# Kernel tuning notes

Measured on AMD Instinct MI355X. Metric: run time of the kernel, lower is better.

Reference implementation:

```python
import jax, jax.numpy as jnp
import numpy as np

B, S, D, H = 8, 1024, 512, 8
HD = D // H
NEG = -1000000000.0
LN_EPS = 1e-5


def setup_inputs() -> dict:
    key = jax.random.key(0)
    ks = jax.random.split(key, 16)
    sc = 0.02
    inp = {
        "query": jax.random.normal(ks[0], (B, S, D), jnp.float32),
        "inputs": jax.random.normal(ks[1], (B, S, D), jnp.float32),
        "ren_mat": jax.random.uniform(ks[2], (B, S, S), jnp.float32) * 5.0,
        "timestamp": jax.random.normal(ks[3], (B, S, S), jnp.float32),
        # causal mask: True where attention is disallowed (strictly upper triangular)
        "mask": jnp.triu(jnp.ones((1, S, S), jnp.bool_), k=1),
        "Wq": jax.random.normal(ks[4], (D, D), jnp.float32) * sc,
        "bq": jnp.zeros((D,), jnp.float32),
        "Wk": jax.random.normal(ks[5], (D, D), jnp.float32) * sc,
        "bk": jnp.zeros((D,), jnp.float32),
        "Wv": jax.random.normal(ks[6], (D, D), jnp.float32) * sc,
        "bv": jnp.zeros((D,), jnp.float32),
        "Wo": jax.random.normal(ks[7], (D, D), jnp.float32) * sc,
        "bo": jnp.zeros((D,), jnp.float32),
        "W1": jax.random.normal(ks[8], (D, D), jnp.float32) * sc,
        "b1": jnp.zeros((D,), jnp.float32),
        "ln_g": jnp.ones((D,), jnp.float32),
        "ln_b": jnp.zeros((D,), jnp.float32),
        "l1": jax.random.uniform(ks[9], (1,), jnp.float32),
    }
    return inp


def reference(query, inputs, ren_mat, timestamp, mask,
              Wq, bq, Wk, bk, Wv, bv, Wo, bo, W1, b1, ln_g, ln_b, l1):
    # QKV projections (qk_same=False path; q,k,v all computed from `inputs`)
    def proj(x, W, b):
        return (x @ W.T + b).reshape(B, S, H, HD).transpose(0, 2, 1, 3)  # (B,H,S,HD)

    q = proj(inputs, Wq, bq)
    k = proj(inputs, Wk, bk)
    v = proj(inputs, Wv, bv)

    m = mask[:, None]  # (1,1,S,S), broadcasts over batch & heads

    scores = jnp.einsum("bhqd,bhkd->bhqk", q, k) / jnp.sqrt(jnp.float32(HD))
    scores = jnp.where(m, NEG, scores)
    prob_attn = jax.nn.softmax(scores, axis=-1)

    # memory blend: log10(ren+1) and exp(-|t|), each masked, summed, softmaxed
    ren_feat = jnp.where(m, NEG, jnp.log10(ren_mat + 1.0)[:, None])      # (B,H,S,S)
    time_stamp = jnp.where(m, NEG, jnp.exp(-jnp.abs(timestamp))[:, None])
    mem_attn = jax.nn.softmax(ren_feat + time_stamp, axis=-1)

    l = l1  # (1,) learned blend coefficient
    prob_attn = (1.0 - l) * prob_attn + l * mem_attn

    out = jnp.einsum("bhqk,bhkd->bhqd", prob_attn, v)
    out = out.transpose(0, 2, 1, 3).reshape(B, S, D)
    out = out @ Wo.T + bo

    # residual FFN + layernorm (dropout disabled / eval mode)
    out = out + (out @ W1.T + b1)
    mu = jnp.mean(out, axis=-1, keepdims=True)
    var = jnp.var(out, axis=-1, keepdims=True)
    out = (out - mu) / jnp.sqrt(var + LN_EPS) * ln_g + ln_b
    return out
```

## Files before the change

### kernel.cpp

```cpp
#include <hip/hip_runtime.h>
#include <math.h>

constexpr int kB = 8, kS = 1024, kD = 512, kH = 8, kHD = 64;
constexpr int kM = kB * kS;

typedef __attribute__((ext_vector_type(8))) short s8v;
typedef __attribute__((ext_vector_type(4))) float f4v;
typedef __attribute__((ext_vector_type(4))) unsigned short u4v;

__device__ __forceinline__ unsigned short f2bf(float f) {
    union { float f; unsigned int u; } c; c.f = f;
    unsigned int u = c.u + 0x7FFFu + ((c.u >> 16) & 1u);
    return (unsigned short)(u >> 16);
}

__device__ __forceinline__ void gl2lds(const unsigned short* g, unsigned short* l) {
    __builtin_amdgcn_global_load_lds(
        (const __attribute__((address_space(1))) unsigned int*)g,
        (__attribute__((address_space(3))) unsigned int*)l, 16, 0, 0);
}

__global__ __launch_bounds__(256) void prep_kernel(
    const float* __restrict__ X, const float* __restrict__ Wq,
    const float* __restrict__ Wk, const float* __restrict__ Wv,
    const float* __restrict__ Wo, const float* __restrict__ W1,
    const float* __restrict__ ren, const float* __restrict__ ts,
    unsigned short* __restrict__ Xbf, unsigned short* __restrict__ Wqkv,
    unsigned short* __restrict__ Wobf, unsigned short* __restrict__ W1bf,
    unsigned short* __restrict__ mem)
{
    __shared__ float red[4];
    const int t = threadIdx.x;
    if (blockIdx.x < 5376) {
        const int idx = blockIdx.x * 256 + t;
        const float* src; unsigned short* dst; int off; bool isw1 = false;
        if (idx < 1048576)      { src = X;  dst = Xbf;           off = idx; }
        else if (idx < 1114112) { src = Wq; dst = Wqkv;          off = idx - 1048576; }
        else if (idx < 1179648) { src = Wk; dst = Wqkv + 262144; off = idx - 1114112; }
        else if (idx < 1245184) { src = Wv; dst = Wqkv + 524288; off = idx - 1179648; }
        else if (idx < 1310720) { src = Wo; dst = Wobf;          off = idx - 1245184; }
        else                    { src = W1; dst = W1bf;          off = idx - 1310720; isw1 = true; }
        float4 v = ((const float4*)src)[off];
        if (isw1) {
            const int e0 = off * 4;
            const int row = e0 >> 9, col0 = e0 & 511;
            if (row >= col0 && row < col0 + 4) ((float*)&v)[row - col0] += 1.0f;
        }
        u4v p;
        p[0] = f2bf(v.x); p[1] = f2bf(v.y); p[2] = f2bf(v.z); p[3] = f2bf(v.w);
        ((u4v*)dst)[off] = p;
        return;
    }
    const int bi = blockIdx.x - 5376;
    const int i = bi & (kS - 1);
    const float* renr = ren + (size_t)bi * kS;
    const float* tsr  = ts  + (size_t)bi * kS;
    unsigned short* memr = mem + (size_t)bi * kS;
    const int j0 = t * 4;
    const float4 r4 = *(const float4*)(renr + j0);
    const float4 t4 = *(const float4*)(tsr + j0);
    float rv[4] = {r4.x, r4.y, r4.z, r4.w};
    float tv[4] = {t4.x, t4.y, t4.z, t4.w};
    float p4[4];
    float lsum = 0.0f;
#pragma unroll
    for (int e = 0; e < 4; ++e) {
        const int j = j0 + e;
        float p = 0.0f;
        if (j <= i) {
            const float val = 0.30102999566f * __log2f(rv[e] + 1.0f) + __expf(-fabsf(tv[e]));
            p = __expf(val);
        }
        p4[e] = p;
        lsum += p;
    }
#pragma unroll
    for (int d = 1; d < 64; d <<= 1) lsum += __shfl_xor(lsum, d);
    if ((t & 63) == 0) red[t >> 6] = lsum;
    __syncthreads();
    const float Z = red[0] + red[1] + red[2] + red[3];
    const float inv = 1.0f / Z;
    u4v pk;
#pragma unroll
    for (int e = 0; e < 4; ++e) pk[e] = f2bf(p4[e] * inv);
    *(u4v*)(memr + j0) = pk;
}

template <int NT>
__device__ __forceinline__ void mfma_core2(
    const unsigned short* __restrict__ A, const unsigned short* __restrict__ B,
    int M0, int N0, unsigned short* As, unsigned short* Bs, f4v (&acc)[4][NT])
{
    const int t = threadIdx.x, w = t >> 6, lane = t & 63;
    const int l16 = lane & 15, quad = lane >> 4;
    const int wm = (w & 1) * 64, wn = (w >> 1) * (NT * 16);
    constexpr int NB = NT / 2;

    const unsigned short* gA[2]; unsigned short* lA[2];
#pragma unroll
    for (int i = 0; i < 2; ++i) {
        const int r0 = w * 32 + i * 16;
        const int r = r0 + (lane >> 2);
        const int c = (lane & 3) ^ ((r >> 1) & 3);
        gA[i] = A + (size_t)(M0 + r) * 512 + c * 8;
        lA[i] = As + r0 * 32;
    }
    const unsigned short* gB[NB]; unsigned short* lB[NB];
#pragma unroll
    for (int i = 0; i < NB; ++i) {
        const int r0 = w * (16 * NB) + i * 16;
        const int r = r0 + (lane >> 2);
        const int c = (lane & 3) ^ ((r >> 1) & 3);
        gB[i] = B + (size_t)(N0 + r) * 512 + c * 8;
        lB[i] = Bs + r0 * 32;
    }

    const f4v zero = {0.0f, 0.0f, 0.0f, 0.0f};
#pragma unroll
    for (int mt = 0; mt < 4; ++mt)
#pragma unroll
        for (int nt = 0; nt < NT; ++nt) acc[mt][nt] = zero;

#pragma unroll 1
    for (int k0 = 0; k0 < 512; k0 += 32) {
        gl2lds(gA[0] + k0, lA[0]);
        gl2lds(gA[1] + k0, lA[1]);
#pragma unroll
        for (int i = 0; i < NB; ++i) gl2lds(gB[i] + k0, lB[i]);
        __syncthreads();
        s8v af[4], bf_[NT];
#pragma unroll
        for (int mt = 0; mt < 4; ++mt) {
            const int r = wm + mt * 16 + l16;
            const int p = r * 4 + (quad ^ ((r >> 1) & 3));
            af[mt] = *(const s8v*)&As[p * 8];
        }
#pragma unroll
        for (int nt = 0; nt < NT; ++nt) {
            const int r = wn + nt * 16 + l16;
            const int p = r * 4 + (quad ^ ((r >> 1) & 3));
            bf_[nt] = *(const s8v*)&Bs[p * 8];
        }
#pragma unroll
        for (int mt = 0; mt < 4; ++mt)
#pragma unroll
            for (int nt = 0; nt < NT; ++nt)
                acc[mt][nt] = __builtin_amdgcn_mfma_f32_16x16x32_bf16(
                    af[mt], bf_[nt], acc[mt][nt], 0, 0, 0);
        __syncthreads();
    }
}

__global__ __launch_bounds__(256) void qkv_mfma_kernel(
    const unsigned short* __restrict__ Xbf, const unsigned short* __restrict__ Wqkv,
    const float* __restrict__ bq, const float* __restrict__ bk, const float* __restrict__ bv,
    unsigned short* __restrict__ qbf, unsigned short* __restrict__ kbf,
    unsigned short* __restrict__ vTbf)
{
    __shared__ __align__(16) unsigned short As[128 * 32];
    __shared__ __align__(16) unsigned short Bs[128 * 32];
    f4v acc[4][4];
    const int y = blockIdx.y;
    const int t = threadIdx.x, w = t >> 6, lane = t & 63;
    const int l16 = lane & 15, quad = lane >> 4;
    const int wm = (w & 1) * 64, wn = (w >> 1) * 64;

    if (y < 8) {
        const int M0 = blockIdx.x * 128, N0 = y * 128;
        mfma_core2<4>(Xbf, Wqkv, M0, N0, As, Bs, acc);
        const int z = N0 >> 9;
        const float* bias = (z == 0) ? bq : bk;
        unsigned short* out = (z == 0) ? qbf : kbf;
#pragma unroll
        for (int nt = 0; nt < 4; ++nt) {
            const int n512 = (N0 + wn + nt * 16 + l16) & 511;
            const int h = n512 >> 6, hd = n512 & 63;
            const float bv_ = bias[n512];
#pragma unroll
            for (int mt = 0; mt < 4; ++mt) {
#pragma unroll
                for (int rr = 0; rr < 4; ++rr) {
                    const int m = M0 + wm + mt * 16 + quad * 4 + rr;
                    const int b = m >> 10, s = m & (kS - 1);
                    out[(((size_t)b * kH + h) * kS + s) * kHD + hd] =
                        f2bf(acc[mt][nt][rr] + bv_);
                }
            }
        }
    } else {
        const int M0 = (y - 8) * 128, N0 = blockIdx.x * 128;
        mfma_core2<4>(Wqkv + (size_t)1024 * 512, Xbf, M0, N0, As, Bs, acc);
#pragma unroll
        for (int mt = 0; mt < 4; ++mt) {
#pragma unroll
            for (int rr = 0; rr < 4; ++rr) {
                const int vcol = M0 + wm + mt * 16 + quad * 4 + rr;
                const int h = vcol >> 6, hd = vcol & 63;
                const float bv_ = bv[vcol];
#pragma unroll
                for (int nt = 0; nt < 4; ++nt) {
                    const int sg = N0 + wn + nt * 16 + l16;
                    const int b = sg >> 10, s = sg & (kS - 1);
                    vTbf[(((size_t)b * kH + h) * kHD + hd) * kS + s] =
                        f2bf(acc[mt][nt][rr] + bv_);
                }
            }
        }
    }
}

__global__ __launch_bounds__(256) void gemm_wo_kernel(
    const unsigned short* __restrict__ Abf, const unsigned short* __restrict__ Wobf,
    const float* __restrict__ bo, unsigned short* __restrict__ out1bf)
{
    __shared__ __align__(16) unsigned short As[128 * 32];
    __shared__ __align__(16) unsigned short Bs[64 * 32];
    f4v acc[4][2];
    const int M0 = blockIdx.x * 128, N0 = blockIdx.y * 64;
    mfma_core2<2>(Abf, Wobf, M0, N0, As, Bs, acc);
    const int t = threadIdx.x, w = t >> 6, lane = t & 63;
    const int l16 = lane & 15, quad = lane >> 4;
    const int wm = (w & 1) * 64, wn = (w >> 1) * 32;
#pragma unroll
    for (int nt = 0; nt < 2; ++nt) {
        const int n = N0 + wn + nt * 16 + l16;
        const float bv_ = bo[n];
#pragma unroll
        for (int mt = 0; mt < 4; ++mt)
#pragma unroll
            for (int rr = 0; rr < 4; ++rr) {
                const int m = M0 + wm + mt * 16 + quad * 4 + rr;
                out1bf[(size_t)m * kD + n] = f2bf(acc[mt][nt][rr] + bv_);
            }
    }
}

__global__ __launch_bounds__(256) void gemm_w1_kernel(
    const unsigned short* __restrict__ Abf, const unsigned short* __restrict__ W1bf,
    const float* __restrict__ b1, float* __restrict__ out)
{
    __shared__ __align__(16) unsigned short As[128 * 32];
    __shared__ __align__(16) unsigned short Bs[64 * 32];
    f4v acc[4][2];
    const int M0 = blockIdx.x * 128, N0 = blockIdx.y * 64;
    mfma_core2<2>(Abf, W1bf, M0, N0, As, Bs, acc);
    const int t = threadIdx.x, w = t >> 6, lane = t & 63;
    const int l16 = lane & 15, quad = lane >> 4;
    const int wm = (w & 1) * 64, wn = (w >> 1) * 32;
#pragma unroll
    for (int nt = 0; nt < 2; ++nt) {
        const int n = N0 + wn + nt * 16 + l16;
        const float bv_ = b1[n];
#pragma unroll
        for (int mt = 0; mt < 4; ++mt)
#pragma unroll
            for (int rr = 0; rr < 4; ++rr) {
                const int m = M0 + wm + mt * 16 + quad * 4 + rr;
                out[(size_t)m * kD + n] = acc[mt][nt][rr] + bv_;
            }
    }
}

#define LDSFRAG(tile, r, c) (*(const s8v*)&(tile)[(size_t)(r) * 64 + ((((c) ^ ((r) & 7))) << 3)])

__global__ __launch_bounds__(256) void flash_attn_kernel(
    const unsigned short* __restrict__ q, const unsigned short* __restrict__ k,
    const unsigned short* __restrict__ vT, const unsigned short* __restrict__ mem,
    const float* __restrict__ l1, unsigned short* __restrict__ aout)
{
    const int qp = blockIdx.x;
    const int hi = 15 - qp, lo = qp;
    const int h = blockIdx.y, b = blockIdx.z;
    const int bh = b * kH + h;
    const int t = threadIdx.x;
    const int w = t >> 6, lane = t & 63;
    const int quad = lane >> 4, l16 = lane & 15;
    const float lam = l1[0];

    __shared__ __align__(16) unsigned short KV[2][2][64 * 64];
    __shared__ __align__(16) unsigned short P_lds[4][16][72];

    const int tbase[2] = {hi * 64, lo * 64};
    s8v qa[2][2];
    const unsigned short* mbase[2];
#pragma unroll
    for (int ti = 0; ti < 2; ++ti) {
        const unsigned short* qrow = q + ((size_t)bh * kS + tbase[ti] + w * 16 + l16) * kHD;
        qa[ti][0] = *(const s8v*)(qrow + quad * 8);
        qa[ti][1] = *(const s8v*)(qrow + 32 + quad * 8);
        mbase[ti] = mem + ((size_t)b * kS + tbase[ti] + w * 16 + l16) * kS;
    }

    const unsigned short* kb = k + (size_t)bh * kS * kHD;
    const unsigned short* vb = vT + (size_t)bh * kHD * kS;

    const unsigned short* gsrc[4];
    int gstep[4];
    unsigned short* ldst[4];
#pragma unroll
    for (int u = 0; u < 4; ++u) {
        const int s = w * 4 + u;
        const int rloc = (s & 7) * 8 + (lane >> 3);
        const int chunk = (lane & 7) ^ ((lane >> 3) & 7);
        if (s < 8) {
            gsrc[u] = kb + (size_t)rloc * kHD + chunk * 8;
            gstep[u] = kHD;
            ldst[u] = &KV[0][0][(size_t)s * 512];
        } else {
            gsrc[u] = vb + (size_t)rloc * kS + chunk * 8;
            gstep[u] = 1;
            ldst[u] = &KV[0][1][(size_t)(s - 8) * 512];
        }
    }

#pragma unroll
    for (int u = 0; u < 4; ++u) gl2lds(gsrc[u], ldst[u]);
    s8v maC[2][2];
#pragma unroll
    for (int ti = 0; ti < 2; ++ti) {
        maC[ti][0] = *(const s8v*)(mbase[ti] + quad * 8);
        maC[ti][1] = *(const s8v*)(mbase[ti] + 32 + quad * 8);
    }

    const f4v zero = {0.0f, 0.0f, 0.0f, 0.0f};
    f4v Oa[2][4], Om[2][4];
    float lr[2][4];
#pragma unroll
    for (int ti = 0; ti < 2; ++ti)
#pragma unroll
        for (int nt = 0; nt < 4; ++nt) {
            Oa[ti][nt] = zero; Om[ti][nt] = zero; lr[ti][nt] = 0.0f;
        }

    for (int kt = 0; kt <= hi; ++kt) {
        __syncthreads();
        const int cur = kt & 1;
        s8v maN[2][2];
        const bool stage_next = (kt < hi);
        if (stage_next) {
            const int jn = (kt + 1) * 64;
            const int boff = ((kt + 1) & 1) * 8192;
#pragma unroll
            for (int u = 0; u < 4; ++u)
                gl2lds(gsrc[u] + (size_t)jn * gstep[u], ldst[u] + boff);
            maN[0][0] = *(const s8v*)(mbase[0] + jn + quad * 8);
            maN[0][1] = *(const s8v*)(mbase[0] + jn + 32 + quad * 8);
            if (kt + 1 <= lo) {
                maN[1][0] = *(const s8v*)(mbase[1] + jn + quad * 8);
                maN[1][1] = *(const s8v*)(mbase[1] + jn + 32 + quad * 8);
            }
        }
        const unsigned short* Kc = &KV[cur][0][0];
        const unsigned short* Vc = &KV[cur][1][0];

        s8v vf[4][2];
#pragma unroll
        for (int nt = 0; nt < 4; ++nt) {
            const int r = nt * 16 + l16;
            vf[nt][0] = LDSFRAG(Vc, r, quad);
            vf[nt][1] = LDSFRAG(Vc, r, 4 + quad);
        }

#pragma unroll
        for (int ti = 0; ti < 2; ++ti) {
            if (ti == 1 && kt > lo) continue;
            const bool diag = (kt == ((ti == 0) ? hi : lo));
#pragma unroll
            for (int ct = 0; ct < 4; ++ct) {
                const int r = ct * 16 + l16;
                const s8v kb0 = LDSFRAG(Kc, r, quad);
                const s8v kb1 = LDSFRAG(Kc, r, 4 + quad);
                f4v acc = zero;
                acc = __builtin_amdgcn_mfma_f32_16x16x32_bf16(qa[ti][0], kb0, acc, 0, 0, 0);
                acc = __builtin_amdgcn_mfma_f32_16x16x32_bf16(qa[ti][1], kb1, acc, 0, 0, 0);
#pragma unroll
                for (int rr = 0; rr < 4; ++rr) {
                    float p = __expf(acc[rr] * 0.125f);
                    if (diag && (ct * 16 + l16) > (w * 16 + quad * 4 + rr)) p = 0.0f;
                    lr[ti][rr] += p;
                    P_lds[w][quad * 4 + rr][ct * 16 + l16] = f2bf(p);
                }
            }
            const s8v pa0 = *(const s8v*)&P_lds[w][l16][quad * 8];
            const s8v pa1 = *(const s8v*)&P_lds[w][l16][32 + quad * 8];
#pragma unroll
            for (int nt = 0; nt < 4; ++nt) {
                Oa[ti][nt] = __builtin_amdgcn_mfma_f32_16x16x32_bf16(pa0, vf[nt][0], Oa[ti][nt], 0, 0, 0);
                Oa[ti][nt] = __builtin_amdgcn_mfma_f32_16x16x32_bf16(pa1, vf[nt][1], Oa[ti][nt], 0, 0, 0);
                Om[ti][nt] = __builtin_amdgcn_mfma_f32_16x16x32_bf16(maC[ti][0], vf[nt][0], Om[ti][nt], 0, 0, 0);
                Om[ti][nt] = __builtin_amdgcn_mfma_f32_16x16x32_bf16(maC[ti][1], vf[nt][1], Om[ti][nt], 0, 0, 0);
            }
        }
        if (stage_next) {
            maC[0][0] = maN[0][0]; maC[0][1] = maN[0][1];
            if (kt + 1 <= lo) { maC[1][0] = maN[1][0]; maC[1][1] = maN[1][1]; }
        }
    }

#pragma unroll
    for (int ti = 0; ti < 2; ++ti) {
        float inv[4];
#pragma unroll
        for (int rr = 0; rr < 4; ++rr) {
            float Z = lr[ti][rr];
            Z += __shfl_xor(Z, 1);
            Z += __shfl_xor(Z, 2);
            Z += __shfl_xor(Z, 4);
            Z += __shfl_xor(Z, 8);
            inv[rr] = (1.0f - lam) / Z;
        }
        const int r0 = tbase[ti] + w * 16;
#pragma unroll
        for (int nt = 0; nt < 4; ++nt)
#pragma unroll
            for (int rr = 0; rr < 4; ++rr) {
                const int i = r0 + quad * 4 + rr;
                const int d = h * kHD + nt * 16 + l16;
                aout[((size_t)b * kS + i) * kD + d] =
                    f2bf(Oa[ti][nt][rr] * inv[rr] + lam * Om[ti][nt][rr]);
            }
    }
}

__global__ __launch_bounds__(256) void ln_kernel(
    const float* __restrict__ x, const float* __restrict__ g,
    const float* __restrict__ bb, float* __restrict__ out)
{
    const int row = blockIdx.x;
    const int t = threadIdx.x;
    const float* xr = x + (size_t)row * kD;
    float a = xr[t], c = xr[t + 256];
    __shared__ float red[256];
    float s1 = a + c, s2 = a * a + c * c;
    red[t] = s1;
    __syncthreads();
    for (int s = 128; s > 0; s >>= 1) {
        if (t < s) red[t] += red[t + s];
        __syncthreads();
    }
    const float sum = red[0];
    __syncthreads();
    red[t] = s2;
    __syncthreads();
    for (int s = 128; s > 0; s >>= 1) {
        if (t < s) red[t] += red[t + s];
        __syncthreads();
    }
    const float sq = red[0];
    float mu = sum * (1.0f / kD);
    float var = sq * (1.0f / kD) - mu * mu;
    float inv = rsqrtf(var + 1e-5f);
    out[(size_t)row * kD + t]       = (a - mu) * inv * g[t] + bb[t];
    out[(size_t)row * kD + t + 256] = (c - mu) * inv * g[t + 256] + bb[t + 256];
}

extern "C" void kernel_launch(void* const* d_in, const int* in_sizes, int n_in,
                              void* d_out, int out_size, void* d_ws, size_t ws_size,
                              hipStream_t stream) {
    const float* X   = (const float*)d_in[1];
    const float* ren = (const float*)d_in[2];
    const float* ts  = (const float*)d_in[3];
    const float* Wq = (const float*)d_in[5];  const float* bq = (const float*)d_in[6];
    const float* Wk = (const float*)d_in[7];  const float* bk = (const float*)d_in[8];
    const float* Wv = (const float*)d_in[9];  const float* bv = (const float*)d_in[10];
    const float* Wo = (const float*)d_in[11]; const float* bo = (const float*)d_in[12];
    const float* W1 = (const float*)d_in[13]; const float* b1 = (const float*)d_in[14];
    const float* lng = (const float*)d_in[15]; const float* lnb = (const float*)d_in[16];
    const float* l1 = (const float*)d_in[17];
    float* out = (float*)d_out;

    char* wsb = (char*)d_ws;
    unsigned short* Xbf    = (unsigned short*)(wsb);
    unsigned short* Wqkvbf = (unsigned short*)(wsb + (8u  << 20));
    unsigned short* Wobf   = (unsigned short*)(wsb + (10u << 20));
    unsigned short* W1bf   = (unsigned short*)(wsb + (11u << 20));
    unsigned short* qbf    = (unsigned short*)(wsb + (12u << 20));
    unsigned short* kbf    = (unsigned short*)(wsb + (20u << 20));
    unsigned short* vTbf   = (unsigned short*)(wsb + (28u << 20));
    unsigned short* membf  = (unsigned short*)(wsb + (36u << 20));
    unsigned short* aoutbf = (unsigned short*)(wsb + (52u << 20));
    unsigned short* out1bf = (unsigned short*)(wsb + (60u << 20));

    prep_kernel<<<dim3(5376 + kB * kS), 256, 0, stream>>>(
        X, Wq, Wk, Wv, Wo, W1, ren, ts, Xbf, Wqkvbf, Wobf, W1bf, membf);
    qkv_mfma_kernel<<<dim3(kM / 128, 12), 256, 0, stream>>>(
        Xbf, Wqkvbf, bq, bk, bv, qbf, kbf, vTbf);
    flash_attn_kernel<<<dim3(8, kH, kB), 256, 0, stream>>>(
        qbf, kbf, vTbf, membf, l1, aoutbf);
    gemm_wo_kernel<<<dim3(kM / 128, kD / 64), 256, 0, stream>>>(
        aoutbf, Wobf, bo, out1bf);
    gemm_w1_kernel<<<dim3(kM / 128, kD / 64), 256, 0, stream>>>(
        out1bf, W1bf, b1, out);
    ln_kernel<<<dim3(kM), 256, 0, stream>>>(out, lng, lnb, out);
}
```

Measured before the change: 283.6 us.

## Fold Wo into W1 algebraically and split attention key loop across wave groups

Precomputes the combined weight (W1+I)·Wo and its bias inside the QKV launch, so the two back-to-back output GEMMs become one GEMM. This removes one GEMM launch and the bf16 round trip of the intermediate activation, at the cost of an extra small weight GEMM and a Wo transpose in prep. Separately, the flash attention kernel goes to 512 threads, with two wave groups each handling alternate key tiles over a 4-deep LDS buffer. Their partial accumulators and row sums are then reduced through LDS, adding parallelism per block but also extra synchronisation and LDS traffic.

```diff
diff --git a/kernel.cpp b/kernel.cpp
--- a/kernel.cpp
+++ b/kernel.cpp
@@ -25,21 +25,21 @@
     const float* __restrict__ Wk, const float* __restrict__ Wv,
     const float* __restrict__ Wo, const float* __restrict__ W1,
     const float* __restrict__ ren, const float* __restrict__ ts,
+    const float* __restrict__ bo_g,
     unsigned short* __restrict__ Xbf, unsigned short* __restrict__ Wqkv,
-    unsigned short* __restrict__ Wobf, unsigned short* __restrict__ W1bf,
+    unsigned short* __restrict__ WoT, unsigned short* __restrict__ W1bf,
     unsigned short* __restrict__ mem)
 {
     __shared__ float red[4];
     const int t = threadIdx.x;
-    if (blockIdx.x < 5376) {
+    if (blockIdx.x < 5120) {
         const int idx = blockIdx.x * 256 + t;
         const float* src; unsigned short* dst; int off; bool isw1 = false;
         if (idx < 1048576)      { src = X;  dst = Xbf;           off = idx; }
         else if (idx < 1114112) { src = Wq; dst = Wqkv;          off = idx - 1048576; }
         else if (idx < 1179648) { src = Wk; dst = Wqkv + 262144; off = idx - 1114112; }
         else if (idx < 1245184) { src = Wv; dst = Wqkv + 524288; off = idx - 1179648; }
-        else if (idx < 1310720) { src = Wo; dst = Wobf;          off = idx - 1245184; }
-        else                    { src = W1; dst = W1bf;          off = idx - 1310720; isw1 = true; }
+        else                    { src = W1; dst = W1bf;          off = idx - 1245184; isw1 = true; }
         float4 v = ((const float4*)src)[off];
         if (isw1) {
             const int e0 = off * 4;
@@ -51,7 +51,34 @@
         ((u4v*)dst)[off] = p;
         return;
     }
-    const int bi = blockIdx.x - 5376;
+    if (blockIdx.x >= 13312) {
+        const int bi2 = blockIdx.x - 13312;
+        if (bi2 < 64) {
+            __shared__ float T[64][65];
+            const int tr = bi2 >> 3, tc = bi2 & 7;
+            const int rr0 = t >> 4, cc0 = (t & 15) * 4;
+#pragma unroll
+            for (int i2 = 0; i2 < 4; ++i2) {
+                const int r = i2 * 16 + rr0;
+                const float4 v = *(const float4*)&Wo[(size_t)(tr * 64 + r) * 512 + tc * 64 + cc0];
+                T[r][cc0] = v.x; T[r][cc0 + 1] = v.y; T[r][cc0 + 2] = v.z; T[r][cc0 + 3] = v.w;
+            }
+            __syncthreads();
+#pragma unroll
+            for (int i2 = 0; i2 < 4; ++i2) {
+                const int r2 = i2 * 16 + rr0;
+                u4v p;
+                p[0] = f2bf(T[cc0][r2]);     p[1] = f2bf(T[cc0 + 1][r2]);
+                p[2] = f2bf(T[cc0 + 2][r2]); p[3] = f2bf(T[cc0 + 3][r2]);
+                *(u4v*)&WoT[(size_t)(tc * 64 + r2) * 512 + tr * 64 + cc0] = p;
+            }
+        } else {
+            WoT[262144 + t]       = f2bf(bo_g[t]);
+            WoT[262144 + 256 + t] = f2bf(bo_g[t + 256]);
+        }
+        return;
+    }
+    const int bi = blockIdx.x - 5120;
     const int i = bi & (kS - 1);
     const float* renr = ren + (size_t)bi * kS;
     const float* tsr  = ts  + (size_t)bi * kS;
@@ -154,17 +181,41 @@
 __global__ __launch_bounds__(256) void qkv_mfma_kernel(
     const unsigned short* __restrict__ Xbf, const unsigned short* __restrict__ Wqkv,
     const float* __restrict__ bq, const float* __restrict__ bk, const float* __restrict__ bv,
+    const unsigned short* __restrict__ W1bf, const unsigned short* __restrict__ WoT,
+    const float* __restrict__ b1,
     unsigned short* __restrict__ qbf, unsigned short* __restrict__ kbf,
-    unsigned short* __restrict__ vTbf)
+    unsigned short* __restrict__ vTbf,
+    unsigned short* __restrict__ Wcomb, float* __restrict__ bcomb)
 {
     __shared__ __align__(16) unsigned short As[128 * 32];
     __shared__ __align__(16) unsigned short Bs[128 * 32];
-    f4v acc[4][4];
     const int y = blockIdx.y;
     const int t = threadIdx.x, w = t >> 6, lane = t & 63;
     const int l16 = lane & 15, quad = lane >> 4;
+
+    if (y == 12) {
+        if (blockIdx.x >= 36) return;
+        f4v acc[4][2];
+        const int M0 = (blockIdx.x / 9) * 128, N0 = (blockIdx.x % 9) * 64;
+        mfma_core2<2>(W1bf, WoT, M0, N0, As, Bs, acc);
+        const int wm = (w & 1) * 64, wn = (w >> 1) * 32;
+#pragma unroll
+        for (int nt = 0; nt < 2; ++nt) {
+            const int qq = N0 + wn + nt * 16 + l16;
+#pragma unroll
+            for (int mt = 0; mt < 4; ++mt)
+#pragma unroll
+                for (int rr = 0; rr < 4; ++rr) {
+                    const int m = M0 + wm + mt * 16 + quad * 4 + rr;
+                    if (qq < 512)       Wcomb[(size_t)m * 512 + qq] = f2bf(acc[mt][nt][rr]);
+                    else if (qq == 512) bcomb[m] = acc[mt][nt][rr] + b1[m];
+                }
+        }
+        return;
+    }
+
+    f4v acc[4][4];
     const int wm = (w & 1) * 64, wn = (w >> 1) * 64;
-
     if (y < 8) {
         const int M0 = blockIdx.x * 128, N0 = y * 128;
         mfma_core2<4>(Xbf, Wqkv, M0, N0, As, Bs, acc);
@@ -209,48 +260,22 @@
     }
 }
 
-__global__ __launch_bounds__(256) void gemm_wo_kernel(
-    const unsigned short* __restrict__ Abf, const unsigned short* __restrict__ Wobf,
-    const float* __restrict__ bo, unsigned short* __restrict__ out1bf)
+__global__ __launch_bounds__(256) void gemm_final_kernel(
+    const unsigned short* __restrict__ Abf, const unsigned short* __restrict__ Wcomb,
+    const float* __restrict__ bcomb, float* __restrict__ out)
 {
     __shared__ __align__(16) unsigned short As[128 * 32];
     __shared__ __align__(16) unsigned short Bs[64 * 32];
     f4v acc[4][2];
     const int M0 = blockIdx.x * 128, N0 = blockIdx.y * 64;
-    mfma_core2<2>(Abf, Wobf, M0, N0, As, Bs, acc);
+    mfma_core2<2>(Abf, Wcomb, M0, N0, As, Bs, acc);
     const int t = threadIdx.x, w = t >> 6, lane = t & 63;
     const int l16 = lane & 15, quad = lane >> 4;
     const int wm = (w & 1) * 64, wn = (w >> 1) * 32;
 #pragma unroll
     for (int nt = 0; nt < 2; ++nt) {
         const int n = N0 + wn + nt * 16 + l16;
-        const float bv_ = bo[n];
-#pragma unroll
-        for (int mt = 0; mt < 4; ++mt)
-#pragma unroll
-            for (int rr = 0; rr < 4; ++rr) {
-                const int m = M0 + wm + mt * 16 + quad * 4 + rr;
-                out1bf[(size_t)m * kD + n] = f2bf(acc[mt][nt][rr] + bv_);
-            }
-    }
-}
-
-__global__ __launch_bounds__(256) void gemm_w1_kernel(
-    const unsigned short* __restrict__ Abf, const unsigned short* __restrict__ W1bf,
-    const float* __restrict__ b1, float* __restrict__ out)
-{
-    __shared__ __align__(16) unsigned short As[128 * 32];
-    __shared__ __align__(16) unsigned short Bs[64 * 32];
-    f4v acc[4][2];
-    const int M0 = blockIdx.x * 128, N0 = blockIdx.y * 64;
-    mfma_core2<2>(Abf, W1bf, M0, N0, As, Bs, acc);
-    const int t = threadIdx.x, w = t >> 6, lane = t & 63;
-    const int l16 = lane & 15, quad = lane >> 4;
-    const int wm = (w & 1) * 64, wn = (w >> 1) * 32;
-#pragma unroll
-    for (int nt = 0; nt < 2; ++nt) {
-        const int n = N0 + wn + nt * 16 + l16;
-        const float bv_ = b1[n];
+        const float bv_ = bcomb[n];
 #pragma unroll
         for (int mt = 0; mt < 4; ++mt)
 #pragma unroll
@@ -263,7 +288,7 @@
 
 #define LDSFRAG(tile, r, c) (*(const s8v*)&(tile)[(size_t)(r) * 64 + ((((c) ^ ((r) & 7))) << 3)])
 
-__global__ __launch_bounds__(256) void flash_attn_kernel(
+__global__ __launch_bounds__(512, 4) void flash_attn_kernel(
     const unsigned short* __restrict__ q, const unsigned short* __restrict__ k,
     const unsigned short* __restrict__ vT, const unsigned short* __restrict__ mem,
     const float* __restrict__ l1, unsigned short* __restrict__ aout)
@@ -273,54 +298,43 @@
     const int h = blockIdx.y, b = blockIdx.z;
     const int bh = b * kH + h;
     const int t = threadIdx.x;
-    const int w = t >> 6, lane = t & 63;
+    const int w = t >> 6, w4 = w & 3, g = w >> 2;
+    const int lane = t & 63;
     const int quad = lane >> 4, l16 = lane & 15;
     const float lam = l1[0];
 
-    __shared__ __align__(16) unsigned short KV[2][2][64 * 64];
-    __shared__ __align__(16) unsigned short P_lds[4][16][72];
+    __shared__ __align__(16) unsigned short KV[4][2][64 * 64];
+    __shared__ __align__(16) unsigned short P_lds[8][16 * 64];
 
     const int tbase[2] = {hi * 64, lo * 64};
     s8v qa[2][2];
     const unsigned short* mbase[2];
 #pragma unroll
     for (int ti = 0; ti < 2; ++ti) {
-        const unsigned short* qrow = q + ((size_t)bh * kS + tbase[ti] + w * 16 + l16) * kHD;
+        const unsigned short* qrow = q + ((size_t)bh * kS + tbase[ti] + w4 * 16 + l16) * kHD;
         qa[ti][0] = *(const s8v*)(qrow + quad * 8);
         qa[ti][1] = *(const s8v*)(qrow + 32 + quad * 8);
-        mbase[ti] = mem + ((size_t)b * kS + tbase[ti] + w * 16 + l16) * kS;
+        mbase[ti] = mem + ((size_t)b * kS + tbase[ti] + w4 * 16 + l16) * kS;
     }
 
     const unsigned short* kb = k + (size_t)bh * kS * kHD;
     const unsigned short* vb = vT + (size_t)bh * kHD * kS;
 
     const unsigned short* gsrc[4];
-    int gstep[4];
-    unsigned short* ldst[4];
+    int gstep[4], loff[4];
 #pragma unroll
     for (int u = 0; u < 4; ++u) {
-        const int s = w * 4 + u;
-        const int rloc = (s & 7) * 8 + (lane >> 3);
+        const int sp = w4 * 4 + u;
+        const int rloc = (sp & 7) * 8 + (lane >> 3);
         const int chunk = (lane & 7) ^ ((lane >> 3) & 7);
-        if (s < 8) {
-            gsrc[u] = kb + (size_t)rloc * kHD + chunk * 8;
-            gstep[u] = kHD;
-            ldst[u] = &KV[0][0][(size_t)s * 512];
-        } else {
-            gsrc[u] = vb + (size_t)rloc * kS + chunk * 8;
-            gstep[u] = 1;
-            ldst[u] = &KV[0][1][(size_t)(s - 8) * 512];
-        }
-    }
-
-#pragma unroll
-    for (int u = 0; u < 4; ++u) gl2lds(gsrc[u], ldst[u]);
-    s8v maC[2][2];
-#pragma unroll
-    for (int ti = 0; ti < 2; ++ti) {
-        maC[ti][0] = *(const s8v*)(mbase[ti] + quad * 8);
-        maC[ti][1] = *(const s8v*)(mbase[ti] + 32 + quad * 8);
-    }
+        if (sp < 8) { gsrc[u] = kb + (size_t)rloc * kHD + chunk * 8; gstep[u] = 64 * kHD; loff[u] = (sp & 7) * 512; }
+        else        { gsrc[u] = vb + (size_t)rloc * kS  + chunk * 8; gstep[u] = 64;       loff[u] = 4096 + (sp & 7) * 512; }
+    }
+    unsigned short* KVf = &KV[0][0][0];
+
+#pragma unroll
+    for (int u = 0; u < 4; ++u)
+        gl2lds(gsrc[u] + (size_t)g * gstep[u], KVf + g * 8192 + loff[u]);
 
     const f4v zero = {0.0f, 0.0f, 0.0f, 0.0f};
     f4v Oa[2][4], Om[2][4];
@@ -332,26 +346,30 @@
             Oa[ti][nt] = zero; Om[ti][nt] = zero; lr[ti][nt] = 0.0f;
         }
 
-    for (int kt = 0; kt <= hi; ++kt) {
-        __syncthreads();
-        const int cur = kt & 1;
-        s8v maN[2][2];
-        const bool stage_next = (kt < hi);
-        if (stage_next) {
-            const int jn = (kt + 1) * 64;
-            const int boff = ((kt + 1) & 1) * 8192;
+    const int nI = hi / 2 + 1;
+    for (int it = 0; it < nI; ++it) {
+        __syncthreads();
+        const int kt = 2 * it + g;
+        const int Tn = 2 * it + 2 + g;
+        if (Tn <= hi) {
 #pragma unroll
             for (int u = 0; u < 4; ++u)
-                gl2lds(gsrc[u] + (size_t)jn * gstep[u], ldst[u] + boff);
-            maN[0][0] = *(const s8v*)(mbase[0] + jn + quad * 8);
-            maN[0][1] = *(const s8v*)(mbase[0] + jn + 32 + quad * 8);
-            if (kt + 1 <= lo) {
-                maN[1][0] = *(const s8v*)(mbase[1] + jn + quad * 8);
-                maN[1][1] = *(const s8v*)(mbase[1] + jn + 32 + quad * 8);
-            }
-        }
-        const unsigned short* Kc = &KV[cur][0][0];
-        const unsigned short* Vc = &KV[cur][1][0];
+                gl2lds(gsrc[u] + (size_t)Tn * gstep[u], KVf + (Tn & 3) * 8192 + loff[u]);
+        }
+        const bool a0 = (kt <= hi);
+        const bool a1 = (kt <= lo);
+        if (!a0) continue;
+
+        const int jn = kt * 64;
+        s8v ma0a, ma0b, ma1a, ma1b;
+        ma0a = *(const s8v*)(mbase[0] + jn + quad * 8);
+        ma0b = *(const s8v*)(mbase[0] + jn + 32 + quad * 8);
+        if (a1) {
+            ma1a = *(const s8v*)(mbase[1] + jn + quad * 8);
+            ma1b = *(const s8v*)(mbase[1] + jn + 32 + quad * 8);
+        }
+        const unsigned short* Kc = &KV[kt & 3][0][0];
+        const unsigned short* Vc = &KV[kt & 3][1][0];
 
         s8v vf[4][2];
 #pragma unroll
@@ -363,7 +381,7 @@
 
 #pragma unroll
         for (int ti = 0; ti < 2; ++ti) {
-            if (ti == 1 && kt > lo) continue;
+            if (ti == 1 && !a1) continue;
             const bool diag = (kt == ((ti == 0) ? hi : lo));
 #pragma unroll
             for (int ct = 0; ct < 4; ++ct) {
@@ -376,25 +394,67 @@
 #pragma unroll
                 for (int rr = 0; rr < 4; ++rr) {
                     float p = __expf(acc[rr] * 0.125f);
-                    if (diag && (ct * 16 + l16) > (w * 16 + quad * 4 + rr)) p = 0.0f;
+                    if (diag && r > (w4 * 16 + quad * 4 + rr)) p = 0.0f;
                     lr[ti][rr] += p;
-                    P_lds[w][quad * 4 + rr][ct * 16 + l16] = f2bf(p);
+                    const int pr = quad * 4 + rr;
+                    P_lds[w][pr * 64 + ((((ct * 2 + (l16 >> 3)) ^ (pr & 7)) << 3) | (l16 & 7))] = f2bf(p);
                 }
             }
-            const s8v pa0 = *(const s8v*)&P_lds[w][l16][quad * 8];
-            const s8v pa1 = *(const s8v*)&P_lds[w][l16][32 + quad * 8];
+            const s8v pa0 = LDSFRAG(&P_lds[w][0], l16, quad);
+            const s8v pa1 = LDSFRAG(&P_lds[w][0], l16, 4 + quad);
+            const s8v m0 = (ti == 0) ? ma0a : ma1a;
+            const s8v m1 = (ti == 0) ? ma0b : ma1b;
 #pragma unroll
             for (int nt = 0; nt < 4; ++nt) {
                 Oa[ti][nt] = __builtin_amdgcn_mfma_f32_16x16x32_bf16(pa0, vf[nt][0], Oa[ti][nt], 0, 0, 0);
                 Oa[ti][nt] = __builtin_amdgcn_mfma_f32_16x16x32_bf16(pa1, vf[nt][1], Oa[ti][nt], 0, 0, 0);
-                Om[ti][nt] = __builtin_amdgcn_mfma_f32_16x16x32_bf16(maC[ti][0], vf[nt][0], Om[ti][nt], 0, 0, 0);
-                Om[ti][nt] = __builtin_amdgcn_mfma_f32_16x16x32_bf16(maC[ti][1], vf[nt][1], Om[ti][nt], 0, 0, 0);
-            }
-        }
-        if (stage_next) {
-            maC[0][0] = maN[0][0]; maC[0][1] = maN[0][1];
-            if (kt + 1 <= lo) { maC[1][0] = maN[1][0]; maC[1][1] = maN[1][1]; }
-        }
+                Om[ti][nt] = __builtin_amdgcn_mfma_f32_16x16x32_bf16(m0, vf[nt][0], Om[ti][nt], 0, 0, 0);
+                Om[ti][nt] = __builtin_amdgcn_mfma_f32_16x16x32_bf16(m1, vf[nt][1], Om[ti][nt], 0, 0, 0);
+            }
+        }
+    }
+
+    float* Pf = (float*)&P_lds[0][0];
+    const int cbase = (w4 * 64 + lane) * 16;
+#pragma unroll
+    for (int ti = 0; ti < 2; ++ti) {
+        __syncthreads();
+        if (g) {
+#pragma unroll
+            for (int nt = 0; nt < 4; ++nt) *(f4v*)&Pf[cbase + nt * 4] = Oa[ti][nt];
+        }
+        __syncthreads();
+        if (!g) {
+#pragma unroll
+            for (int nt = 0; nt < 4; ++nt) Oa[ti][nt] += *(const f4v*)&Pf[cbase + nt * 4];
+        }
+        __syncthreads();
+        if (g) {
+#pragma unroll
+            for (int nt = 0; nt < 4; ++nt) *(f4v*)&Pf[cbase + nt * 4] = Om[ti][nt];
+        }
+        __syncthreads();
+        if (!g) {
+#pragma unroll
+            for (int nt = 0; nt < 4; ++nt) Om[ti][nt] += *(const f4v*)&Pf[cbase + nt * 4];
+        }
+    }
+    __syncthreads();
+    if (g) {
+        const int lbase = (w4 * 64 + lane) * 8;
+#pragma unroll
+        for (int ti = 0; ti < 2; ++ti)
+#pragma unroll
+            for (int rr = 0; rr < 4; ++rr) Pf[lbase + ti * 4 + rr] = lr[ti][rr];
+    }
+    __syncthreads();
+    if (g) return;
+    {
+        const int lbase = (w4 * 64 + lane) * 8;
+#pragma unroll
+        for (int ti = 0; ti < 2; ++ti)
+#pragma unroll
+            for (int rr = 0; rr < 4; ++rr) lr[ti][rr] += Pf[lbase + ti * 4 + rr];
     }
 
 #pragma unroll
@@ -409,7 +469,7 @@
             Z += __shfl_xor(Z, 8);
             inv[rr] = (1.0f - lam) / Z;
         }
-        const int r0 = tbase[ti] + w * 16;
+        const int r0 = tbase[ti] + w4 * 16;
 #pragma unroll
         for (int nt = 0; nt < 4; ++nt)
 #pragma unroll
@@ -472,24 +532,23 @@
     char* wsb = (char*)d_ws;
     unsigned short* Xbf    = (unsigned short*)(wsb);
     unsigned short* Wqkvbf = (unsigned short*)(wsb + (8u  << 20));
-    unsigned short* Wobf   = (unsigned short*)(wsb + (10u << 20));
+    unsigned short* WoTbf  = (unsigned short*)(wsb + (10u << 20));
     unsigned short* W1bf   = (unsigned short*)(wsb + (11u << 20));
     unsigned short* qbf    = (unsigned short*)(wsb + (12u << 20));
     unsigned short* kbf    = (unsigned short*)(wsb + (20u << 20));
     unsigned short* vTbf   = (unsigned short*)(wsb + (28u << 20));
     unsigned short* membf  = (unsigned short*)(wsb + (36u << 20));
     unsigned short* aoutbf = (unsigned short*)(wsb + (52u << 20));
-    unsigned short* out1bf = (unsigned short*)(wsb + (60u << 20));
-
-    prep_kernel<<<dim3(5376 + kB * kS), 256, 0, stream>>>(
-        X, Wq, Wk, Wv, Wo, W1, ren, ts, Xbf, Wqkvbf, Wobf, W1bf, membf);
-    qkv_mfma_kernel<<<dim3(kM / 128, 12), 256, 0, stream>>>(
-        Xbf, Wqkvbf, bq, bk, bv, qbf, kbf, vTbf);
-    flash_attn_kernel<<<dim3(8, kH, kB), 256, 0, stream>>>(
+    unsigned short* Wcombf = (unsigned short*)(wsb + (60u << 20));
+    float*          bcombf = (float*)        (wsb + (61u << 20));
+
+    prep_kernel<<<dim3(13377), 256, 0, stream>>>(
+        X, Wq, Wk, Wv, Wo, W1, ren, ts, bo, Xbf, Wqkvbf, WoTbf, W1bf, membf);
+    qkv_mfma_kernel<<<dim3(kM / 128, 13), 256, 0, stream>>>(
+        Xbf, Wqkvbf, bq, bk, bv, W1bf, WoTbf, b1, qbf, kbf, vTbf, Wcombf, bcombf);
+    flash_attn_kernel<<<dim3(8, kH, kB), 512, 0, stream>>>(
         qbf, kbf, vTbf, membf, l1, aoutbf);
-    gemm_wo_kernel<<<dim3(kM / 128, kD / 64), 256, 0, stream>>>(
-        aoutbf, Wobf, bo, out1bf);
-    gemm_w1_kernel<<<dim3(kM / 128, kD / 64), 256, 0, stream>>>(
-        out1bf, W1bf, b1, out);
+    gemm_final_kernel<<<dim3(kM / 128, kD / 64), 256, 0, stream>>>(
+        aoutbf, Wcombf, bcombf, out);
     ln_kernel<<<dim3(kM), 256, 0, stream>>>(out, lng, lnb, out);
 }
```

After: 368.8 us. 30.0% more time.
